# Kernel tuning notes

Measured on AMD Instinct MI355X. Metric: run time of the kernel, lower is better.

## Reference

```python
import jax, jax.numpy as jnp
import numpy as np

EPS = 1e-12

def softmax_mask(x, mask, axis):
    # stable masked softmax: exp(x - max) * mask / (sum + eps)
    shift = jnp.max(x, axis=axis, keepdims=True)
    e = jnp.exp(x - shift) * mask
    return e / (jnp.sum(e, axis=axis, keepdims=True) + EPS)

def setup_inputs() -> dict:
    key = jax.random.key(0)
    kq, kk, kv, km = jax.random.split(key, 4)
    B, Lq, Lk, d, dv = 16, 2048, 2048, 128, 128
    q = jax.random.normal(kq, (B, Lq, d), dtype=jnp.float32)
    k = jax.random.normal(kk, (B, Lk, d), dtype=jnp.float32)
    v = jax.random.normal(kv, (B, Lk, dv), dtype=jnp.float32)
    mask = (jax.random.uniform(km, (B, Lq, Lk)) > 0.1).astype(jnp.float32)
    return {"q": q, "k": k, "v": v, "mask": mask}

def reference(q, k, v, mask):
    # attn[b,i,j] = q[b,i,:] . k[b,j,:]
    attn = jnp.einsum('bqd,bkd->bqk', q, k)
    col_attn = softmax_mask(attn, mask, axis=1)  # normalize over queries (columns)
    row_attn = softmax_mask(attn, mask, axis=2)  # normalize over keys (rows)
    gated = col_attn * row_attn
    output = jnp.einsum('bqk,bkd->bqd', gated, v)
    return (output, gated)
```

## Files before the change

### kernel.cpp

```cpp
#include <hip/hip_runtime.h>

#define BATCH 16
#define LSEQ  2048
#define DDIM  128
#define EPSV  1e-12f
#define NTILE (LSEQ / 64)
#define NROWS (BATCH * LSEQ)

typedef __attribute__((ext_vector_type(4))) float f32x4;
typedef __attribute__((ext_vector_type(8))) __bf16 bf16x8;
typedef __attribute__((ext_vector_type(8))) unsigned short u16x8;

__device__ __forceinline__ unsigned short f2bf(float x) {
    unsigned int u = __float_as_uint(x);
    u += 0x7FFFu + ((u >> 16) & 1u);
    return (unsigned short)(u >> 16);
}
__device__ __forceinline__ float bf2f(unsigned short h) {
    return __uint_as_float(((unsigned int)h) << 16);
}

__device__ __forceinline__ int swz(int row, int col8) {
    return (row << 6) + ((((col8 >> 3) ^ row) & 7) << 3);
}

__global__ __launch_bounds__(256, 2) void k1_qk_stats(
    const float* __restrict__ q, const float* __restrict__ kmat,
    const float* __restrict__ mask, float* __restrict__ attn,
    float* __restrict__ rowMt, float* __restrict__ rowSt,
    float* __restrict__ colMt, float* __restrict__ colSt)
{
    const int b  = blockIdx.z;
    const int it = blockIdx.y * 128;
    const int jt = blockIdx.x * 128;

    __shared__ __attribute__((aligned(16))) unsigned short smem[4 * 128 * 64];
    unsigned short* Ah = smem;
    unsigned short* Al = smem + 128 * 64;
    unsigned short* Bh = smem + 2 * 128 * 64;
    unsigned short* Bl = smem + 3 * 128 * 64;

    const int tid  = threadIdx.x;
    const int lane = tid & 63;
    const int w    = tid >> 6;
    const int wrow = (w >> 1) << 6;
    const int wcol = (w & 1) << 6;
    const int g    = lane >> 4;
    const int cl   = lane & 15;

    const float* qb = q    + ((size_t)b * LSEQ + it) * DDIM;
    const float* kb = kmat + ((size_t)b * LSEQ + jt) * DDIM;

    const int lr = tid >> 2;
    const int lc = (tid & 3) << 4;

    f32x4 acc[4][4];
    const f32x4 zero = {0.f, 0.f, 0.f, 0.f};
#pragma unroll
    for (int i = 0; i < 4; ++i)
#pragma unroll
        for (int j = 0; j < 4; ++j) acc[i][j] = zero;

    for (int ks2 = 0; ks2 < DDIM; ks2 += 64) {
        if (ks2) __syncthreads();
#pragma unroll
        for (int pr = 0; pr < 2; ++pr) {
            const int row = lr + (pr << 6);
            const float* qr = qb + (size_t)row * DDIM + ks2 + lc;
            const float* kr = kb + (size_t)row * DDIM + ks2 + lc;
#pragma unroll
            for (int cc = 0; cc < 16; cc += 8) {
                float xs[8], ys[8];
                *(float4*)&xs[0] = *(const float4*)(qr + cc);
                *(float4*)&xs[4] = *(const float4*)(qr + cc + 4);
                *(float4*)&ys[0] = *(const float4*)(kr + cc);
                *(float4*)&ys[4] = *(const float4*)(kr + cc + 4);
                u16x8 qh, ql, kh, kl;
#pragma unroll
                for (int e = 0; e < 8; ++e) {
                    const unsigned short h0 = f2bf(xs[e]);
                    qh[e] = h0;
                    ql[e] = f2bf(xs[e] - bf2f(h0));
                    const unsigned short h1 = f2bf(ys[e]);
                    kh[e] = h1;
                    kl[e] = f2bf(ys[e] - bf2f(h1));
                }
                const int o = swz(row, lc + cc);
                *(u16x8*)&Ah[o] = qh;
                *(u16x8*)&Al[o] = ql;
                *(u16x8*)&Bh[o] = kh;
                *(u16x8*)&Bl[o] = kl;
            }
        }
        __syncthreads();

#pragma unroll
        for (int ks = 0; ks < 64; ks += 32) {
            const int colb = ks + (g << 3);
            bf16x8 ah[4], al[4], bh[4], bl[4];
#pragma unroll
            for (int f = 0; f < 4; ++f) {
                const int ra = wrow + (f << 4) + cl;
                const int rb = wcol + (f << 4) + cl;
                ah[f] = __builtin_bit_cast(bf16x8, *(const u16x8*)&Ah[swz(ra, colb)]);
                al[f] = __builtin_bit_cast(bf16x8, *(const u16x8*)&Al[swz(ra, colb)]);
                bh[f] = __builtin_bit_cast(bf16x8, *(const u16x8*)&Bh[swz(rb, colb)]);
                bl[f] = __builtin_bit_cast(bf16x8, *(const u16x8*)&Bl[swz(rb, colb)]);
            }
#pragma unroll
            for (int fr = 0; fr < 4; ++fr)
#pragma unroll
                for (int fc = 0; fc < 4; ++fc) {
                    acc[fr][fc] = __builtin_amdgcn_mfma_f32_16x16x32_bf16(ah[fr], bh[fc], acc[fr][fc], 0, 0, 0);
                    acc[fr][fc] = __builtin_amdgcn_mfma_f32_16x16x32_bf16(ah[fr], bl[fc], acc[fr][fc], 0, 0, 0);
                    acc[fr][fc] = __builtin_amdgcn_mfma_f32_16x16x32_bf16(al[fr], bh[fc], acc[fr][fc], 0, 0, 0);
                }
        }
    }

    const size_t grow0 = (size_t)b * LSEQ + it + wrow;
    float*       arow  = attn + grow0 * LSEQ + jt + wcol;
    const float* mrow  = mask + grow0 * LSEQ + jt + wcol;

    float colm[4];
#pragma unroll
    for (int fc = 0; fc < 4; ++fc) {
        float m = acc[0][fc][0];
#pragma unroll
        for (int fr = 0; fr < 4; ++fr)
#pragma unroll
            for (int r = 0; r < 4; ++r) m = fmaxf(m, acc[fr][fc][r]);
        m = fmaxf(m, __shfl_xor(m, 16, 64));
        m = fmaxf(m, __shfl_xor(m, 32, 64));
        colm[fc] = m;
    }
    float rowm[4][4];
#pragma unroll
    for (int fr = 0; fr < 4; ++fr)
#pragma unroll
        for (int r = 0; r < 4; ++r) {
            float m = fmaxf(fmaxf(acc[fr][0][r], acc[fr][1][r]),
                            fmaxf(acc[fr][2][r], acc[fr][3][r]));
            m = fmaxf(m, __shfl_xor(m, 1, 64));
            m = fmaxf(m, __shfl_xor(m, 2, 64));
            m = fmaxf(m, __shfl_xor(m, 4, 64));
            m = fmaxf(m, __shfl_xor(m, 8, 64));
            rowm[fr][r] = m;
        }

    float cols_[4] = {0.f, 0.f, 0.f, 0.f};
    float rows_[4][4];
#pragma unroll
    for (int fr = 0; fr < 4; ++fr) {
#pragma unroll
        for (int r = 0; r < 4; ++r) {
            const int R = (fr << 4) + (g << 2) + r;
            float rs = 0.f;
#pragma unroll
            for (int fc = 0; fc < 4; ++fc) {
                const int C = (fc << 4) + cl;
                const float x = acc[fr][fc][r];
                arow[(size_t)R * LSEQ + C] = x;
                const float mk = mrow[(size_t)R * LSEQ + C];
                rs        += __expf(x - rowm[fr][r]) * mk;
                cols_[fc] += __expf(x - colm[fc])    * mk;
            }
            rs += __shfl_xor(rs, 1, 64);
            rs += __shfl_xor(rs, 2, 64);
            rs += __shfl_xor(rs, 4, 64);
            rs += __shfl_xor(rs, 8, 64);
            rows_[fr][r] = rs;
        }
    }
#pragma unroll
    for (int fc = 0; fc < 4; ++fc) {
        float s = cols_[fc];
        s += __shfl_xor(s, 16, 64);
        s += __shfl_xor(s, 32, 64);
        cols_[fc] = s;
    }

    const int ti = (blockIdx.y << 1) + (w >> 1);
    const int tj = (blockIdx.x << 1) + (w & 1);
    if (cl == 0) {
        const size_t rbase = (size_t)tj * NROWS + (size_t)b * LSEQ + it + wrow;
#pragma unroll
        for (int fr = 0; fr < 4; ++fr)
#pragma unroll
            for (int r = 0; r < 4; ++r) {
                const int R = (fr << 4) + (g << 2) + r;
                rowMt[rbase + R] = rowm[fr][r];
                rowSt[rbase + R] = rows_[fr][r];
            }
    }
    if (g == 0) {
        const size_t cbase = (size_t)ti * NROWS + (size_t)b * LSEQ + jt + wcol;
#pragma unroll
        for (int fc = 0; fc < 4; ++fc) {
            colMt[cbase + (fc << 4) + cl] = colm[fc];
            colSt[cbase + (fc << 4) + cl] = cols_[fc];
        }
    }
}

__global__ __launch_bounds__(256) void k2_combine(
    const float* __restrict__ rowMt, const float* __restrict__ rowSt,
    const float* __restrict__ colMt, const float* __restrict__ colSt,
    float* __restrict__ rmaxf, float* __restrict__ rsumf,
    float* __restrict__ cmaxf, float* __restrict__ csumf)
{
    const int id = blockIdx.x * 256 + threadIdx.x;
    const bool isRow = (id < NROWS);
    const int off = isRow ? id : id - NROWS;
    const float* Mt = isRow ? rowMt : colMt;
    const float* St = isRow ? rowSt : colSt;

    float m = -INFINITY;
#pragma unroll
    for (int t = 0; t < NTILE; ++t) m = fmaxf(m, Mt[(size_t)t * NROWS + off]);
    float s = 0.f;
#pragma unroll
    for (int t = 0; t < NTILE; ++t)
        s += St[(size_t)t * NROWS + off] * __expf(Mt[(size_t)t * NROWS + off] - m);

    if (isRow) { rmaxf[off] = m; rsumf[off] = s; }
    else       { cmaxf[off] = m; csumf[off] = s; }
}

__global__ __launch_bounds__(256) void k3_gated_out(
    const float* __restrict__ mask, const float* __restrict__ v,
    const float* __restrict__ rmaxf, const float* __restrict__ cmaxf,
    const float* __restrict__ rsumf, const float* __restrict__ csumf,
    float* __restrict__ gated, float* __restrict__ outp)
{
    const int b   = blockIdx.y;
    const int it0 = blockIdx.x * 32;

    __shared__ float Gs[32][36];
    __shared__ float Vs[32][128];
    __shared__ float RowM[32], RowIS[32];
    __shared__ float ColM[32], ColIS[32];

    const int tid = threadIdx.x;
    if (tid < 32) {
        RowM[tid]  = rmaxf[b * LSEQ + it0 + tid];
        RowIS[tid] = 1.f / (rsumf[b * LSEQ + it0 + tid] + EPSV);
    }

    const int r0  = (tid >> 5) << 2;
    const int c0  = (tid & 31) << 2;
    const int gr  = tid >> 3;
    const int gc4 = (tid & 7) << 2;
    const int vr  = tid >> 5;
    const int vc  = (tid & 31) << 2;

    float acc[4][4];
#pragma unroll
    for (int u = 0; u < 4; ++u)
#pragma unroll
        for (int w = 0; w < 4; ++w) acc[u][w] = 0.f;

    const float* mb = mask  + ((size_t)b * LSEQ + it0) * LSEQ;
    float*       gb = gated + ((size_t)b * LSEQ + it0) * LSEQ;
    const float* vb = v + (size_t)b * LSEQ * DDIM;

    float4 xpre = *(const float4*)(gb + (size_t)gr * LSEQ + gc4);
    float4 mpre = *(const float4*)(mb + (size_t)gr * LSEQ + gc4);

    for (int j0 = 0; j0 < LSEQ; j0 += 32) {
        __syncthreads();
        if (tid < 32) {
            ColM[tid]  = cmaxf[b * LSEQ + j0 + tid];
            ColIS[tid] = 1.f / (csumf[b * LSEQ + j0 + tid] + EPSV);
        }
#pragma unroll
        for (int p = 0; p < 4; ++p) {
            const int row = vr + p * 8;
            *(float4*)&Vs[row][vc] = *(const float4*)(vb + (size_t)(j0 + row) * DDIM + vc);
        }
        __syncthreads();

        float4 xc = xpre, mk = mpre;
        if (j0 + 32 < LSEQ) {
            xpre = *(const float4*)(gb + (size_t)gr * LSEQ + j0 + 32 + gc4);
            mpre = *(const float4*)(mb + (size_t)gr * LSEQ + j0 + 32 + gc4);
        }
        {
            const float mrw = RowM[gr], isr = RowIS[gr];
            float g0 = mk.x * __expf(2.f * xc.x - mrw - ColM[gc4 + 0]) * isr * ColIS[gc4 + 0];
            float g1 = mk.y * __expf(2.f * xc.y - mrw - ColM[gc4 + 1]) * isr * ColIS[gc4 + 1];
            float g2 = mk.z * __expf(2.f * xc.z - mrw - ColM[gc4 + 2]) * isr * ColIS[gc4 + 2];
            float g3 = mk.w * __expf(2.f * xc.w - mrw - ColM[gc4 + 3]) * isr * ColIS[gc4 + 3];
            *(float4*)(gb + (size_t)gr * LSEQ + j0 + gc4) = make_float4(g0, g1, g2, g3);
            Gs[gc4 + 0][gr] = g0; Gs[gc4 + 1][gr] = g1;
            Gs[gc4 + 2][gr] = g2; Gs[gc4 + 3][gr] = g3;
        }
        __syncthreads();
#pragma unroll
        for (int kk = 0; kk < 32; ++kk) {
            float4 a4 = *(const float4*)&Gs[kk][r0];
            float4 b4 = *(const float4*)&Vs[kk][c0];
            float av[4] = {a4.x, a4.y, a4.z, a4.w};
            float bv[4] = {b4.x, b4.y, b4.z, b4.w};
#pragma unroll
            for (int u = 0; u < 4; ++u)
#pragma unroll
                for (int w = 0; w < 4; ++w)
                    acc[u][w] = fmaf(av[u], bv[w], acc[u][w]);
        }
    }

    float* ob = outp + ((size_t)b * LSEQ + it0) * DDIM;
#pragma unroll
    for (int u = 0; u < 4; ++u)
        *(float4*)(ob + (size_t)(r0 + u) * DDIM + c0) =
            make_float4(acc[u][0], acc[u][1], acc[u][2], acc[u][3]);
}

extern "C" void kernel_launch(void* const* d_in, const int* in_sizes, int n_in,
                              void* d_out, int out_size, void* d_ws, size_t ws_size,
                              hipStream_t stream)
{
    (void)in_sizes; (void)n_in; (void)out_size; (void)ws_size;
    const float* q    = (const float*)d_in[0];
    const float* k    = (const float*)d_in[1];
    const float* v    = (const float*)d_in[2];
    const float* mask = (const float*)d_in[3];

    float* outp  = (float*)d_out;
    float* gated = (float*)d_out + (size_t)BATCH * LSEQ * DDIM;

    float* rowMt = (float*)d_ws;
    float* rowSt = rowMt + (size_t)NTILE * NROWS;
    float* colMt = rowSt + (size_t)NTILE * NROWS;
    float* colSt = colMt + (size_t)NTILE * NROWS;
    float* rmaxf = colSt + (size_t)NTILE * NROWS;
    float* rsumf = rmaxf + NROWS;
    float* cmaxf = rsumf + NROWS;
    float* csumf = cmaxf + NROWS;

    dim3 g1(LSEQ / 128, LSEQ / 128, BATCH);
    k1_qk_stats<<<g1, dim3(256), 0, stream>>>(q, k, mask, gated,
                                              rowMt, rowSt, colMt, colSt);

    k2_combine<<<dim3(2 * NROWS / 256), dim3(256), 0, stream>>>(
        rowMt, rowSt, colMt, colSt, rmaxf, rsumf, cmaxf, csumf);

    dim3 g3(LSEQ / 32, BATCH);
    k3_gated_out<<<g3, dim3(256), 0, stream>>>(mask, v, rmaxf, cmaxf,
                                               rsumf, csumf, gated, outp);
}
```

Measured before the change: 814.8 us.

## Run gated·V product on bf16 MFMA with split hi/lo precision and pre-transposed V

Adds a prepass kernel that transposes V and splits it into high and low bf16 halves. The gated-output kernel now also splits each gated tile into bf16 hi/lo, stores it in swizzled shared memory, and computes G·V with three bf16 MFMA products per fragment instead of scalar FP32 FMAs. The output tile grows from 32 to 64 rows. The aim is to move the second matmul off the scalar ALUs and onto the matrix cores while keeping near-FP32 accuracy. The cost is an extra kernel launch, extra workspace traffic for the split V, and a small precision loss from the three-term approximation.

```diff
diff --git a/kernel.cpp b/kernel.cpp
--- a/kernel.cpp
+++ b/kernel.cpp
@@ -22,6 +22,44 @@
 
 __device__ __forceinline__ int swz(int row, int col8) {
     return (row << 6) + ((((col8 >> 3) ^ row) & 7) << 3);
+}
+
+__global__ __launch_bounds__(256) void k0_vtrans(
+    const float* __restrict__ v,
+    unsigned short* __restrict__ vth, unsigned short* __restrict__ vtl)
+{
+    const int b  = blockIdx.z;
+    const int j0 = blockIdx.x * 64;
+    const int d0 = blockIdx.y * 64;
+    __shared__ float T[64][65];
+
+    const int tid = threadIdx.x;
+    {
+        const int jr = tid >> 4;
+        const int c4 = (tid & 15) << 2;
+#pragma unroll
+        for (int p = 0; p < 4; ++p) {
+            const int row = jr + (p << 4);
+            *(float4*)&T[row][c4] =
+                *(const float4*)(v + ((size_t)b * LSEQ + j0 + row) * DDIM + d0 + c4);
+        }
+    }
+    __syncthreads();
+
+    const int dr = tid >> 2;
+    const int jc = (tid & 3) << 4;
+    u16x8 h[2], l[2];
+#pragma unroll
+    for (int e = 0; e < 16; ++e) {
+        const float x = T[jc + e][dr];
+        const unsigned short hh = f2bf(x);
+        h[e >> 3][e & 7] = hh;
+        l[e >> 3][e & 7] = f2bf(x - bf2f(hh));
+    }
+    unsigned short* oh = vth + ((size_t)b * DDIM + d0 + dr) * LSEQ + j0 + jc;
+    unsigned short* ol = vtl + ((size_t)b * DDIM + d0 + dr) * LSEQ + j0 + jc;
+    *(u16x8*)oh = h[0]; *(u16x8*)(oh + 8) = h[1];
+    *(u16x8*)ol = l[0]; *(u16x8*)(ol + 8) = l[1];
 }
 
 __global__ __launch_bounds__(256, 2) void k1_qk_stats(
@@ -227,94 +265,141 @@
     else       { cmaxf[off] = m; csumf[off] = s; }
 }
 
-__global__ __launch_bounds__(256) void k3_gated_out(
-    const float* __restrict__ mask, const float* __restrict__ v,
+__global__ __launch_bounds__(256, 2) void k3_gated_out(
+    const float* __restrict__ mask,
+    const unsigned short* __restrict__ vth, const unsigned short* __restrict__ vtl,
     const float* __restrict__ rmaxf, const float* __restrict__ cmaxf,
     const float* __restrict__ rsumf, const float* __restrict__ csumf,
     float* __restrict__ gated, float* __restrict__ outp)
 {
     const int b   = blockIdx.y;
-    const int it0 = blockIdx.x * 32;
-
-    __shared__ float Gs[32][36];
-    __shared__ float Vs[32][128];
-    __shared__ float RowM[32], RowIS[32];
-    __shared__ float ColM[32], ColIS[32];
-
-    const int tid = threadIdx.x;
-    if (tid < 32) {
+    const int it0 = blockIdx.x * 64;
+
+    __shared__ __attribute__((aligned(16))) unsigned short Gh[64 * 64];
+    __shared__ __attribute__((aligned(16))) unsigned short Gl[64 * 64];
+    __shared__ __attribute__((aligned(16))) unsigned short Vh[128 * 64];
+    __shared__ __attribute__((aligned(16))) unsigned short Vl[128 * 64];
+    __shared__ float RowM[64], RowIS[64], ColM[64], ColIS[64];
+
+    const int tid  = threadIdx.x;
+    const int lane = tid & 63;
+    const int w    = tid >> 6;
+    const int g    = lane >> 4;
+    const int cl   = lane & 15;
+
+    if (tid < 64) {
         RowM[tid]  = rmaxf[b * LSEQ + it0 + tid];
         RowIS[tid] = 1.f / (rsumf[b * LSEQ + it0 + tid] + EPSV);
     }
 
-    const int r0  = (tid >> 5) << 2;
-    const int c0  = (tid & 31) << 2;
-    const int gr  = tid >> 3;
-    const int gc4 = (tid & 7) << 2;
-    const int vr  = tid >> 5;
-    const int vc  = (tid & 31) << 2;
-
-    float acc[4][4];
-#pragma unroll
-    for (int u = 0; u < 4; ++u)
-#pragma unroll
-        for (int w = 0; w < 4; ++w) acc[u][w] = 0.f;
-
+    const int grow = tid >> 2;
+    const int gcb  = (tid & 3) << 4;
+    const int vrow = tid >> 1;
+    const int vcb  = (tid & 1) << 5;
+
+    float*       gb = gated + ((size_t)b * LSEQ + it0) * LSEQ;
     const float* mb = mask  + ((size_t)b * LSEQ + it0) * LSEQ;
-    float*       gb = gated + ((size_t)b * LSEQ + it0) * LSEQ;
-    const float* vb = v + (size_t)b * LSEQ * DDIM;
-
-    float4 xpre = *(const float4*)(gb + (size_t)gr * LSEQ + gc4);
-    float4 mpre = *(const float4*)(mb + (size_t)gr * LSEQ + gc4);
-
-    for (int j0 = 0; j0 < LSEQ; j0 += 32) {
+    const unsigned short* vhb = vth + ((size_t)b * DDIM + vrow) * LSEQ;
+    const unsigned short* vlb = vtl + ((size_t)b * DDIM + vrow) * LSEQ;
+
+    f32x4 acc[4][2];
+    const f32x4 zero = {0.f, 0.f, 0.f, 0.f};
+#pragma unroll
+    for (int i = 0; i < 4; ++i) { acc[i][0] = zero; acc[i][1] = zero; }
+
+    float4 xr[4], mr[4];
+#pragma unroll
+    for (int p = 0; p < 4; ++p) {
+        xr[p] = *(const float4*)(gb + (size_t)grow * LSEQ + gcb + p * 4);
+        mr[p] = *(const float4*)(mb + (size_t)grow * LSEQ + gcb + p * 4);
+    }
+
+#pragma unroll 1
+    for (int j0 = 0; j0 < LSEQ; j0 += 64) {
         __syncthreads();
-        if (tid < 32) {
+        if (tid < 64) {
             ColM[tid]  = cmaxf[b * LSEQ + j0 + tid];
             ColIS[tid] = 1.f / (csumf[b * LSEQ + j0 + tid] + EPSV);
         }
 #pragma unroll
+        for (int cc = 0; cc < 32; cc += 8) {
+            *(u16x8*)&Vh[swz(vrow, vcb + cc)] = *(const u16x8*)(vhb + j0 + vcb + cc);
+            *(u16x8*)&Vl[swz(vrow, vcb + cc)] = *(const u16x8*)(vlb + j0 + vcb + cc);
+        }
+        __syncthreads();
+
+        const float mrw = RowM[grow], isr = RowIS[grow];
+        float gs[16];
+#pragma unroll
         for (int p = 0; p < 4; ++p) {
-            const int row = vr + p * 8;
-            *(float4*)&Vs[row][vc] = *(const float4*)(vb + (size_t)(j0 + row) * DDIM + vc);
+            const float xs[4] = {xr[p].x, xr[p].y, xr[p].z, xr[p].w};
+            const float ms[4] = {mr[p].x, mr[p].y, mr[p].z, mr[p].w};
+#pragma unroll
+            for (int e = 0; e < 4; ++e) {
+                const int c = gcb + p * 4 + e;
+                gs[p * 4 + e] = ms[e] * __expf(2.f * xs[e] - mrw - ColM[c]) * isr * ColIS[c];
+            }
+            *(float4*)(gb + (size_t)grow * LSEQ + j0 + gcb + p * 4) =
+                make_float4(gs[p * 4], gs[p * 4 + 1], gs[p * 4 + 2], gs[p * 4 + 3]);
+        }
+#pragma unroll
+        for (int cc = 0; cc < 16; cc += 8) {
+            u16x8 hh, ll;
+#pragma unroll
+            for (int e = 0; e < 8; ++e) {
+                const unsigned short hb = f2bf(gs[cc + e]);
+                hh[e] = hb;
+                ll[e] = f2bf(gs[cc + e] - bf2f(hb));
+            }
+            *(u16x8*)&Gh[swz(grow, gcb + cc)] = hh;
+            *(u16x8*)&Gl[swz(grow, gcb + cc)] = ll;
+        }
+        if (j0 + 64 < LSEQ) {
+#pragma unroll
+            for (int p = 0; p < 4; ++p) {
+                xr[p] = *(const float4*)(gb + (size_t)grow * LSEQ + j0 + 64 + gcb + p * 4);
+                mr[p] = *(const float4*)(mb + (size_t)grow * LSEQ + j0 + 64 + gcb + p * 4);
+            }
         }
         __syncthreads();
 
-        float4 xc = xpre, mk = mpre;
-        if (j0 + 32 < LSEQ) {
-            xpre = *(const float4*)(gb + (size_t)gr * LSEQ + j0 + 32 + gc4);
-            mpre = *(const float4*)(mb + (size_t)gr * LSEQ + j0 + 32 + gc4);
-        }
-        {
-            const float mrw = RowM[gr], isr = RowIS[gr];
-            float g0 = mk.x * __expf(2.f * xc.x - mrw - ColM[gc4 + 0]) * isr * ColIS[gc4 + 0];
-            float g1 = mk.y * __expf(2.f * xc.y - mrw - ColM[gc4 + 1]) * isr * ColIS[gc4 + 1];
-            float g2 = mk.z * __expf(2.f * xc.z - mrw - ColM[gc4 + 2]) * isr * ColIS[gc4 + 2];
-            float g3 = mk.w * __expf(2.f * xc.w - mrw - ColM[gc4 + 3]) * isr * ColIS[gc4 + 3];
-            *(float4*)(gb + (size_t)gr * LSEQ + j0 + gc4) = make_float4(g0, g1, g2, g3);
-            Gs[gc4 + 0][gr] = g0; Gs[gc4 + 1][gr] = g1;
-            Gs[gc4 + 2][gr] = g2; Gs[gc4 + 3][gr] = g3;
-        }
-        __syncthreads();
-#pragma unroll
-        for (int kk = 0; kk < 32; ++kk) {
-            float4 a4 = *(const float4*)&Gs[kk][r0];
-            float4 b4 = *(const float4*)&Vs[kk][c0];
-            float av[4] = {a4.x, a4.y, a4.z, a4.w};
-            float bv[4] = {b4.x, b4.y, b4.z, b4.w};
-#pragma unroll
-            for (int u = 0; u < 4; ++u)
-#pragma unroll
-                for (int w = 0; w < 4; ++w)
-                    acc[u][w] = fmaf(av[u], bv[w], acc[u][w]);
-        }
-    }
-
-    float* ob = outp + ((size_t)b * LSEQ + it0) * DDIM;
-#pragma unroll
-    for (int u = 0; u < 4; ++u)
-        *(float4*)(ob + (size_t)(r0 + u) * DDIM + c0) =
-            make_float4(acc[u][0], acc[u][1], acc[u][2], acc[u][3]);
+#pragma unroll
+        for (int ks = 0; ks < 64; ks += 32) {
+            const int colb = ks + (g << 3);
+            bf16x8 ah[4], al[4], bh[2], bl[2];
+#pragma unroll
+            for (int f = 0; f < 4; ++f) {
+                const int ra = (f << 4) + cl;
+                ah[f] = __builtin_bit_cast(bf16x8, *(const u16x8*)&Gh[swz(ra, colb)]);
+                al[f] = __builtin_bit_cast(bf16x8, *(const u16x8*)&Gl[swz(ra, colb)]);
+            }
+#pragma unroll
+            for (int f = 0; f < 2; ++f) {
+                const int rb = (w << 5) + (f << 4) + cl;
+                bh[f] = __builtin_bit_cast(bf16x8, *(const u16x8*)&Vh[swz(rb, colb)]);
+                bl[f] = __builtin_bit_cast(bf16x8, *(const u16x8*)&Vl[swz(rb, colb)]);
+            }
+#pragma unroll
+            for (int fr = 0; fr < 4; ++fr)
+#pragma unroll
+                for (int fc = 0; fc < 2; ++fc) {
+                    acc[fr][fc] = __builtin_amdgcn_mfma_f32_16x16x32_bf16(ah[fr], bh[fc], acc[fr][fc], 0, 0, 0);
+                    acc[fr][fc] = __builtin_amdgcn_mfma_f32_16x16x32_bf16(al[fr], bh[fc], acc[fr][fc], 0, 0, 0);
+                    acc[fr][fc] = __builtin_amdgcn_mfma_f32_16x16x32_bf16(ah[fr], bl[fc], acc[fr][fc], 0, 0, 0);
+                }
+        }
+    }
+
+    float* ob = outp + ((size_t)b * LSEQ + it0) * DDIM + (w << 5);
+#pragma unroll
+    for (int fr = 0; fr < 4; ++fr)
+#pragma unroll
+        for (int r = 0; r < 4; ++r) {
+            const int R = (fr << 4) + (g << 2) + r;
+#pragma unroll
+            for (int fc = 0; fc < 2; ++fc)
+                ob[(size_t)R * DDIM + (fc << 4) + cl] = acc[fr][fc][r];
+        }
 }
 
 extern "C" void kernel_launch(void* const* d_in, const int* in_sizes, int n_in,
@@ -338,6 +423,11 @@
     float* rsumf = rmaxf + NROWS;
     float* cmaxf = rsumf + NROWS;
     float* csumf = cmaxf + NROWS;
+    unsigned short* vth = (unsigned short*)(csumf + NROWS);
+    unsigned short* vtl = vth + (size_t)BATCH * DDIM * LSEQ;
+
+    dim3 g0(LSEQ / 64, DDIM / 64, BATCH);
+    k0_vtrans<<<g0, dim3(256), 0, stream>>>(v, vth, vtl);
 
     dim3 g1(LSEQ / 128, LSEQ / 128, BATCH);
     k1_qk_stats<<<g1, dim3(256), 0, stream>>>(q, k, mask, gated,
@@ -346,7 +436,7 @@
     k2_combine<<<dim3(2 * NROWS / 256), dim3(256), 0, stream>>>(
         rowMt, rowSt, colMt, colSt, rmaxf, rsumf, cmaxf, csumf);
 
-    dim3 g3(LSEQ / 32, BATCH);
-    k3_gated_out<<<g3, dim3(256), 0, stream>>>(mask, v, rmaxf, cmaxf,
+    dim3 g3(LSEQ / 64, BATCH);
+    k3_gated_out<<<g3, dim3(256), 0, stream>>>(mask, vth, vtl, rmaxf, cmaxf,
                                                rsumf, csumf, gated, outp);
 }
```

Result: faster. 751.3 us (-7.8%).
